# Kernel tuning notes

Hardware: AMD Instinct MI355X
Metric: run time of the kernel (lower is better)

Reference implementation:

```python
import jax, jax.numpy as jnp
import numpy as np

NB, NC, NT = 64, 128, 6
NEURON = (25, 50, 100)
AXIS = 4
EPS = 1e-12


def _offdiag_idx(nc):
    # static [nc, nc-1] column indices of the off-diagonal entries per row
    idx = np.tile(np.arange(nc)[None, :], (nc, 1))
    mask = ~np.eye(nc, dtype=bool)
    return idx[mask].reshape(nc, nc - 1)


def setup_inputs() -> dict:
    key = jax.random.key(0)
    ks = jax.random.split(key, 8)
    P = NT * NT
    coords = jax.random.normal(ks[0], (NB, NC, 3), dtype=jnp.float32)
    atom_types = jax.random.randint(ks[1], (NC,), 0, NT)
    dims = [1] + list(NEURON)
    inp = {"coords": coords, "atom_types": atom_types}
    for i in range(3):
        bound = 1.0 / float(np.sqrt(dims[i]))
        inp[f"W{i+1}"] = jax.random.uniform(ks[2 + 2 * i], (P, dims[i + 1], dims[i]), jnp.float32, -bound, bound)
        inp[f"b{i+1}"] = jax.random.uniform(ks[3 + 2 * i], (P, dims[i + 1]), jnp.float32, -bound, bound)
    return inp


def _channel_dense(x, W, b, channels, res_mode):
    # x: [nb, Ppairs, in]; W[channels]: [Ppairs, out, in] (redundant per-pair gather, as in torch)
    y = jnp.einsum('bpi,poi->bpo', x, W[channels]) + b[channels]
    y = jnp.tanh(y)
    if res_mode == 1:
        y = y + x
    elif res_mode == 2:
        y = y + jnp.concatenate([x, x], axis=-1)
    return y


def _forward(coords, atom_types, W1, b1, W2, b2, W3, b3):
    nb, nc, _ = coords.shape
    idx = jnp.asarray(_offdiag_idx(nc))  # [nc, nc-1], static
    row = jnp.arange(nc)[:, None]

    rij = coords[:, :, None, :] - coords[:, None, :, :]          # [nb,nc,nc,3]
    rij = rij[:, row, idx]                                       # [nb,nc,nc-1,3] off-diagonal
    dij = jnp.linalg.norm(rij, axis=-1)                          # [nb,nc,nc-1]
    dinv = 1.0 / jnp.maximum(dij, EPS)
    loc_env_r = dinv
    loc_env_a = rij * (dinv * dinv)[..., None]                   # [nb,nc,nc-1,3]

    neighbor_types = atom_types[idx]                             # [nc,nc-1]
    channels = (atom_types[:, None] * NT + neighbor_types).reshape(-1)  # [nc*(nc-1)]

    x = loc_env_r.reshape(nb, -1, 1)                             # [nb,P,1]
    y = _channel_dense(x, W1, b1, channels, res_mode=0)          # 1 -> 25
    y = _channel_dense(y, W2, b2, channels, res_mode=2)          # 25 -> 50 (+concat res)
    y = _channel_dense(y, W3, b3, channels, res_mode=2)          # 50 -> 100 (+concat res)

    out = y.reshape(nb, nc, nc - 1, NEURON[-1])                  # [nb,nc,k,100]
    t1 = jnp.einsum('bnka,bnkf->bnaf', loc_env_a, out[..., :AXIS])   # [nb,nc,3,4]
    t2 = jnp.einsum('bnka,bnaf->bnkf', loc_env_a, t1)                # [nb,nc,k,4]
    res = jnp.einsum('bnkg,bnkf->bngf', out, t2)                     # [nb,nc,100,4]
    return res.reshape(nb, nc, -1)


def reference(coords, atom_types, W1, b1, W2, b2, W3, b3):
    return _forward(coords, atom_types, W1, b1, W2, b2, W3, b3)
```

## Files before the change

kernel.cpp:

```cpp
#include <hip/hip_runtime.h>

#define NBATCH 64
#define NCH    128
#define NTYPE  6
#define NK     127
#define N1     25
#define N2     50
#define N3     100
#define NAXIS  4
#define OUTPER 400
#define W2P    28
#define MAXKP  152
#define MAXC4  38

#define R5(M)  M(0) M(1) M(2) M(3) M(4)
#define R7(M)  M(0) M(1) M(2) M(3) M(4) M(5) M(6)
#define R12(M) M(0) M(1) M(2) M(3) M(4) M(5) M(6) M(7) M(8) M(9) M(10) M(11)
#define R25(M) M(0) M(1) M(2) M(3) M(4) M(5) M(6) M(7) M(8) M(9) M(10) M(11) M(12) \
               M(13) M(14) M(15) M(16) M(17) M(18) M(19) M(20) M(21) M(22) M(23) M(24)
#define R25A(M,a) M(a,0) M(a,1) M(a,2) M(a,3) M(a,4) M(a,5) M(a,6) M(a,7) M(a,8) M(a,9) \
               M(a,10) M(a,11) M(a,12) M(a,13) M(a,14) M(a,15) M(a,16) M(a,17) M(a,18) \
               M(a,19) M(a,20) M(a,21) M(a,22) M(a,23) M(a,24)
#define R50(M) R25(M) M(25) M(26) M(27) M(28) M(29) M(30) M(31) M(32) M(33) M(34) \
               M(35) M(36) M(37) M(38) M(39) M(40) M(41) M(42) M(43) M(44) M(45) \
               M(46) M(47) M(48) M(49)

__device__ __forceinline__ float tanh_fast(float x) {
    float e = __expf(2.0f * x);
    return 1.0f - 2.0f * __builtin_amdgcn_rcpf(e + 1.0f);
}

__global__ void k_transpose(const float* __restrict__ coords, float* __restrict__ ct) {
    int t = blockIdx.x * blockDim.x + threadIdx.x;
    if (t >= NBATCH * NCH * 3) return;
    int b  = t & (NBATCH - 1);
    int jd = t >> 6;
    int d  = jd % 3;
    int j  = jd / 3;
    ct[t] = coords[(b * NCH + j) * 3 + d];
}

__device__ __forceinline__ void sort_k_by_type(
    const int* __restrict__ types, int n, int* tysh, int* ks, int* bins, int tid, int nthr)
{
    for (int t = tid; t < NCH; t += nthr) tysh[t] = types[t];
    __syncthreads();
    if (tid == 0) {
        for (int t = 0; t < NTYPE; ++t) bins[t] = 0;
        for (int k = 0; k < NK; ++k) { int j = (k < n) ? k : k + 1; bins[tysh[j]]++; }
        int off = 0;
        for (int t = 0; t < NTYPE; ++t) { int c = bins[t]; bins[t] = off; off += c; }
        for (int k = 0; k < NK; ++k) { int j = (k < n) ? k : k + 1; ks[bins[tysh[j]]++] = k; }
    }
    __syncthreads();
}

__device__ __forceinline__ void sort_pad(
    const int* __restrict__ types, int n, int* tysh, int* ksp, int* chs, int* aux,
    int tid, int nthr)
{
    for (int t = tid; t < NCH; t += nthr) tysh[t] = types[t];
    __syncthreads();
    if (tid == 0) {
        int cnt[NTYPE], pos[NTYPE];
        for (int t = 0; t < NTYPE; ++t) cnt[t] = 0;
        for (int k = 0; k < NK; ++k) { int j = (k < n) ? k : k + 1; cnt[tysh[j]]++; }
        int c = 0;
        for (int t = 0; t < NTYPE; ++t) {
            pos[t] = c;
            int pc = (cnt[t] + 3) & ~3;
            for (int q = c >> 2; q < (c + pc) >> 2; ++q) chs[q] = t;
            for (int p = c + cnt[t]; p < c + pc; ++p) ksp[p] = -1;
            c += pc;
        }
        aux[0] = c >> 2;
        for (int k = 0; k < NK; ++k) { int j = (k < n) ? k : k + 1; ksp[pos[tysh[j]]++] = k; }
    }
    __syncthreads();
}

__global__ __launch_bounds__(256, 4) void k_mlp(
    const float* __restrict__ ct, const int* __restrict__ types,
    const float* __restrict__ W1, const float* __restrict__ B1,
    const float* __restrict__ W2, const float* __restrict__ B2,
    const float* __restrict__ W3, const float* __restrict__ B3,
    float* __restrict__ t1buf)
{
    __shared__ int ks[NK];
    __shared__ int tysh[NCH];
    __shared__ int bins[NTYPE];

    const int n  = blockIdx.x >> 2;
    const int qc = blockIdx.x & 3;
    const int w  = threadIdx.x >> 6;
    const int b  = threadIdx.x & 63;
    const int k0 = qc * 32 + w * 8;

    sort_k_by_type(types, n, tysh, ks, bins, threadIdx.x, 256);

    const float cx = ct[(n*3+0)*NBATCH + b];
    const float cy = ct[(n*3+1)*NBATCH + b];
    const float cz = ct[(n*3+2)*NBATCH + b];
    const int tn = __builtin_amdgcn_readfirstlane(tysh[n]);

    float t1a[12];
#define TIN(i) t1a[i] = 0.0f;
    R12(TIN)
#undef TIN

    for (int kk = 0; kk < 8; ++kk) {
        const int kidx = k0 + kk;
        if (kidx >= NK) break;
        const int sk = __builtin_amdgcn_readfirstlane(ks[kidx]);
        const int j  = (sk < n) ? sk : sk + 1;
        const int ch = __builtin_amdgcn_readfirstlane(tn * NTYPE + tysh[j]);

        const float dx = cx - ct[(j*3+0)*NBATCH + b];
        const float dy = cy - ct[(j*3+1)*NBATCH + b];
        const float dz = cz - ct[(j*3+2)*NBATCH + b];
        const float d2 = dx*dx + dy*dy + dz*dz;
        const float dd = sqrtf(d2);
        const float dinv = __builtin_amdgcn_rcpf(fmaxf(dd, 1e-12f));
        const float di2 = dinv * dinv;
        const float ax = dx * di2, ay = dy * di2, az = dz * di2;

        const float* w1r = W1 + ch * N1;
        const float* b1r = B1 + ch * N1;
        float y1[N1];
#define L1S(o) y1[o] = tanh_fast(fmaf(dinv, w1r[o], b1r[o]));
        R25(L1S)
#undef L1S

        const float* w2r = W2 + ch * (N2 * N1);
        const float* b2r = B2 + ch * N2;
        const float* w3r = W3 + ch * (N3 * N2);
        float zf[4];
        zf[0] = B3[ch*N3+0]; zf[1] = B3[ch*N3+1];
        zf[2] = B3[ch*N3+2]; zf[3] = B3[ch*N3+3];
        float r[4];
#define MLP2I(o,i) z = fmaf(w2r[(o)*N1+(i)], y1[i], z);
#define MLP2(o) { float z = b2r[o]; R25A(MLP2I,o) \
        float y2o = tanh_fast(z) + y1[(o)%N1]; \
        if ((o) < 4) r[(o)&3] = y2o; \
        zf[0] = fmaf(w3r[0*N2+(o)], y2o, zf[0]); \
        zf[1] = fmaf(w3r[1*N2+(o)], y2o, zf[1]); \
        zf[2] = fmaf(w3r[2*N2+(o)], y2o, zf[2]); \
        zf[3] = fmaf(w3r[3*N2+(o)], y2o, zf[3]); }
        R50(MLP2)
#undef MLP2
#undef MLP2I

#define O4F(f) { float o4 = tanh_fast(zf[f]) + r[f]; \
        t1a[0+(f)] = fmaf(ax, o4, t1a[0+(f)]); \
        t1a[4+(f)] = fmaf(ay, o4, t1a[4+(f)]); \
        t1a[8+(f)] = fmaf(az, o4, t1a[8+(f)]); }
        O4F(0) O4F(1) O4F(2) O4F(3)
#undef O4F
    }

    float* dst = t1buf + (n * 12) * NBATCH + b;
#define TAT(i) atomicAdd(dst + (i) * NBATCH, t1a[i]);
    R12(TAT)
#undef TAT
}

__global__ __launch_bounds__(512, 3) void k_res2(
    const float* __restrict__ ct, const int* __restrict__ types,
    const float* __restrict__ W1, const float* __restrict__ B1,
    const float* __restrict__ W2, const float* __restrict__ B2,
    const float* __restrict__ W3, const float* __restrict__ B3,
    const float* __restrict__ t1buf, float* __restrict__ out)
{
    __shared__ float y2t[4 * N2 * NBATCH];
    __shared__ float t2s[4 * NBATCH * NAXIS];
    __shared__ float w2s[N2 * W2P];
    __shared__ float w1s[N1], b1s[N1], b2s[N2];
    __shared__ int   ksp[MAXKP];
    __shared__ int   chs[MAXC4];
    __shared__ int   tysh[NCH];
    __shared__ int   aux[1];

    const int n    = blockIdx.x >> 2;
    const int gh   = (blockIdx.x >> 1) & 1;
    const int kh   = blockIdx.x & 1;
    const int w    = threadIdx.x >> 6;
    const int lane = threadIdx.x & 63;
    const int kk2  = w >> 1;
    const int h    = w & 1;
    const int tid  = threadIdx.x;

    sort_pad(types, n, tysh, ksp, chs, aux, tid, 512);
    const int nch4 = __builtin_amdgcn_readfirstlane(aux[0]);
    const int c_lo = kh ? (nch4 >> 1) : 0;
    const int c_hi = kh ? nch4 : (nch4 >> 1);

    const int tn = __builtin_amdgcn_readfirstlane(tysh[n]);

    float t1r[12];
#define T1L(i) t1r[i] = t1buf[(n*12 + (i))*NBATCH + lane];
    R12(T1L)
#undef T1L

    const int g0 = __builtin_amdgcn_readfirstlane(w * 7);
    int gg[7];
#define GGI(gi) gg[gi] = ((g0 + (gi)) < N2) ? (g0 + (gi)) : (N2 - 1);
    R7(GGI)
#undef GGI

    float racc[7][4];
#define RIN(gi) racc[gi][0]=0.f; racc[gi][1]=0.f; racc[gi][2]=0.f; racc[gi][3]=0.f;
    R7(RIN)
#undef RIN

    float b3v[7];
    int prevty = -1;

    for (int kc = c_lo; kc < c_hi; ++kc) {
        const int tj = __builtin_amdgcn_readfirstlane(chs[kc]);
        const int ch = tn * NTYPE + tj;
        if (tj != prevty) {
            for (int idx = tid; idx < N2*N1; idx += 512)
                w2s[(idx / N1) * W2P + (idx % N1)] = W2[ch*(N2*N1) + idx];
            if (tid < N1) { w1s[tid] = W1[ch*N1+tid]; b1s[tid] = B1[ch*N1+tid]; }
            if (tid < N2) b2s[tid] = B2[ch*N2+tid];
#define B3L(gi) b3v[gi] = B3[ch*N3 + gh*N2 + gg[gi]];
            R7(B3L)
#undef B3L
            prevty = tj;
            __syncthreads();
        }
        const int kb = kc * 4;
        {
            const int sk = __builtin_amdgcn_readfirstlane(ksp[kb + kk2]);
            if (sk >= 0) {
                const int j = (sk < n) ? sk : sk + 1;
                const float dx = ct[(n*3+0)*NBATCH + lane] - ct[(j*3+0)*NBATCH + lane];
                const float dy = ct[(n*3+1)*NBATCH + lane] - ct[(j*3+1)*NBATCH + lane];
                const float dz = ct[(n*3+2)*NBATCH + lane] - ct[(j*3+2)*NBATCH + lane];
                const float d2 = dx*dx + dy*dy + dz*dz;
                const float dd = sqrtf(d2);
                const float dinv = __builtin_amdgcn_rcpf(fmaxf(dd, 1e-12f));

                if (h == 0) {
                    const float di2 = dinv * dinv;
                    const float ax = dx * di2, ay = dy * di2, az = dz * di2;
#define T2W(f) t2s[(kk2*NBATCH + lane)*NAXIS + (f)] = \
                    ax*t1r[f] + ay*t1r[4+(f)] + az*t1r[8+(f)];
                    T2W(0) T2W(1) T2W(2) T2W(3)
#undef T2W
                }

                float y1[N1];
#define L1S(o) y1[o] = tanh_fast(fmaf(dinv, w1s[o], b1s[o]));
                R25(L1S)
#undef L1S
                const int ob = h * N1;
                float* y2w = &y2t[(kk2*N2 + ob)*NBATCH + lane];
#define P1Q(oi,q) { float4 wq = *(const float4*)&w2s[(ob+(oi))*W2P + (q)*4]; \
                    z = fmaf(wq.x, y1[(q)*4+0], z); z = fmaf(wq.y, y1[(q)*4+1], z); \
                    z = fmaf(wq.z, y1[(q)*4+2], z); z = fmaf(wq.w, y1[(q)*4+3], z); }
#define P1S(oi) { float z = b2s[ob+(oi)]; \
                  P1Q(oi,0) P1Q(oi,1) P1Q(oi,2) P1Q(oi,3) P1Q(oi,4) P1Q(oi,5) \
                  z = fmaf(w2s[(ob+(oi))*W2P + 24], y1[24], z); \
                  y2w[(oi)*NBATCH] = tanh_fast(z) + y1[oi]; }
                R25(P1S)
#undef P1S
#undef P1Q
            }
        }
        __syncthreads();
        const float* w3b = W3 + ch * (N3*N2) + (gh*N2) * N2;
        for (int kp = 0; kp < 2; ++kp) {
            const int skA = __builtin_amdgcn_readfirstlane(ksp[kb + kp*2 + 0]);
            const int skB = __builtin_amdgcn_readfirstlane(ksp[kb + kp*2 + 1]);
            if (skA < 0 && skB < 0) continue;
            const float* y2A = &y2t[((kp*2+0)*N2)*NBATCH + lane];
            const float* y2B = &y2t[((kp*2+1)*N2)*NBATCH + lane];
            float zA[7], zB[7];
#define ZIN(gi) zA[gi] = b3v[gi]; zB[gi] = b3v[gi];
            R7(ZIN)
#undef ZIN
            for (int ic = 0; ic < 10; ++ic) {
                const int io = ic * 5;
                float w35[7][5];
#define W35L(gi) w35[gi][0]=w3b[gg[gi]*N2+io+0]; w35[gi][1]=w3b[gg[gi]*N2+io+1]; \
                 w35[gi][2]=w3b[gg[gi]*N2+io+2]; w35[gi][3]=w3b[gg[gi]*N2+io+3]; \
                 w35[gi][4]=w3b[gg[gi]*N2+io+4];
                R7(W35L)
#undef W35L
                if (skA >= 0) {
                    float yv[5];
#define LDA(i) yv[i] = y2A[(io + (i))*NBATCH];
                    R5(LDA)
#undef LDA
#define FA(gi) zA[gi]=fmaf(w35[gi][0],yv[0],zA[gi]); zA[gi]=fmaf(w35[gi][1],yv[1],zA[gi]); \
               zA[gi]=fmaf(w35[gi][2],yv[2],zA[gi]); zA[gi]=fmaf(w35[gi][3],yv[3],zA[gi]); \
               zA[gi]=fmaf(w35[gi][4],yv[4],zA[gi]);
                    R7(FA)
#undef FA
                }
                if (skB >= 0) {
                    float yv[5];
#define LDB(i) yv[i] = y2B[(io + (i))*NBATCH];
                    R5(LDB)
#undef LDB
#define FB(gi) zB[gi]=fmaf(w35[gi][0],yv[0],zB[gi]); zB[gi]=fmaf(w35[gi][1],yv[1],zB[gi]); \
               zB[gi]=fmaf(w35[gi][2],yv[2],zB[gi]); zB[gi]=fmaf(w35[gi][3],yv[3],zB[gi]); \
               zB[gi]=fmaf(w35[gi][4],yv[4],zB[gi]);
                    R7(FB)
#undef FB
                }
            }
            if (skA >= 0) {
                const float4 t2v = *(const float4*)&t2s[((kp*2+0)*NBATCH + lane)*NAXIS];
#define PFA(gi) { float o3 = tanh_fast(zA[gi]) + y2A[gg[gi]*NBATCH]; \
                  racc[gi][0] = fmaf(o3, t2v.x, racc[gi][0]); \
                  racc[gi][1] = fmaf(o3, t2v.y, racc[gi][1]); \
                  racc[gi][2] = fmaf(o3, t2v.z, racc[gi][2]); \
                  racc[gi][3] = fmaf(o3, t2v.w, racc[gi][3]); }
                R7(PFA)
#undef PFA
            }
            if (skB >= 0) {
                const float4 t2v = *(const float4*)&t2s[((kp*2+1)*NBATCH + lane)*NAXIS];
#define PFB(gi) { float o3 = tanh_fast(zB[gi]) + y2B[gg[gi]*NBATCH]; \
                  racc[gi][0] = fmaf(o3, t2v.x, racc[gi][0]); \
                  racc[gi][1] = fmaf(o3, t2v.y, racc[gi][1]); \
                  racc[gi][2] = fmaf(o3, t2v.z, racc[gi][2]); \
                  racc[gi][3] = fmaf(o3, t2v.w, racc[gi][3]); }
                R7(PFB)
#undef PFB
            }
        }
        __syncthreads();
    }

#define PST(gi) if (g0 + (gi) < N2) { \
        float* dp = &out[(lane*NCH + n)*OUTPER + (gh*N2 + g0 + (gi))*NAXIS]; \
        atomicAdd(dp + 0, racc[gi][0]); \
        atomicAdd(dp + 1, racc[gi][1]); \
        atomicAdd(dp + 2, racc[gi][2]); \
        atomicAdd(dp + 3, racc[gi][3]); }
    R7(PST)
#undef PST
}

extern "C" void kernel_launch(void* const* d_in, const int* in_sizes, int n_in,
                              void* d_out, int out_size, void* d_ws, size_t ws_size,
                              hipStream_t stream) {
    const float* coords = (const float*)d_in[0];
    const int*   types  = (const int*)d_in[1];
    const float* W1 = (const float*)d_in[2];
    const float* B1 = (const float*)d_in[3];
    const float* W2 = (const float*)d_in[4];
    const float* B2 = (const float*)d_in[5];
    const float* W3 = (const float*)d_in[6];
    const float* B3 = (const float*)d_in[7];
    float* out = (float*)d_out;

    float* t1buf = (float*)d_ws;
    float* ct    = t1buf + NCH * 12 * NBATCH;

    hipMemsetAsync(t1buf, 0, (size_t)NCH * 12 * NBATCH * sizeof(float), stream);
    hipMemsetAsync(out, 0, (size_t)out_size * sizeof(float), stream);

    k_transpose<<<(NBATCH*NCH*3 + 255)/256, 256, 0, stream>>>(coords, ct);
    k_mlp <<<NCH*4, 256, 0, stream>>>(ct, types, W1,B1,W2,B2,W3,B3, t1buf);
    k_res2<<<NCH*4, 512, 0, stream>>>(ct, types, W1,B1,W2,B2,W3,B3, t1buf, out);
}
```

Before: 829.2 us.

## Process four neighbors per W3 load with float4-packed y2 layout in layer 3

```diff
diff --git a/kernel.cpp b/kernel.cpp
--- a/kernel.cpp
+++ b/kernel.cpp
@@ -12,6 +12,7 @@
 #define W2P    28
 #define MAXKP  152
 #define MAXC4  38
+#define NQ     13
 
 #define R5(M)  M(0) M(1) M(2) M(3) M(4)
 #define R7(M)  M(0) M(1) M(2) M(3) M(4) M(5) M(6)
@@ -164,14 +165,14 @@
 #undef TAT
 }
 
-__global__ __launch_bounds__(512, 3) void k_res2(
+__global__ __launch_bounds__(512, 4) void k_res2(
     const float* __restrict__ ct, const int* __restrict__ types,
     const float* __restrict__ W1, const float* __restrict__ B1,
     const float* __restrict__ W2, const float* __restrict__ B2,
     const float* __restrict__ W3, const float* __restrict__ B3,
     const float* __restrict__ t1buf, float* __restrict__ out)
 {
-    __shared__ float y2t[4 * N2 * NBATCH];
+    __shared__ float y2t[4 * NQ * NBATCH * 4];
     __shared__ float t2s[4 * NBATCH * NAXIS];
     __shared__ float w2s[N2 * W2P];
     __shared__ float w1s[N1], b1s[N1], b2s[N2];
@@ -179,6 +180,8 @@
     __shared__ int   chs[MAXC4];
     __shared__ int   tysh[NCH];
     __shared__ int   aux[1];
+
+#define Y2I(k,q,b,j) ((((k)*NQ + (q))*NBATCH + (b))*4 + (j))
 
     const int n    = blockIdx.x >> 2;
     const int gh   = (blockIdx.x >> 1) & 1;
@@ -195,6 +198,10 @@
     const int c_hi = kh ? nch4 : (nch4 >> 1);
 
     const int tn = __builtin_amdgcn_readfirstlane(tysh[n]);
+
+    const float cx = ct[(n*3+0)*NBATCH + lane];
+    const float cy = ct[(n*3+1)*NBATCH + lane];
+    const float cz = ct[(n*3+2)*NBATCH + lane];
 
     float t1r[12];
 #define T1L(i) t1r[i] = t1buf[(n*12 + (i))*NBATCH + lane];
@@ -234,9 +241,9 @@
             const int sk = __builtin_amdgcn_readfirstlane(ksp[kb + kk2]);
             if (sk >= 0) {
                 const int j = (sk < n) ? sk : sk + 1;
-                const float dx = ct[(n*3+0)*NBATCH + lane] - ct[(j*3+0)*NBATCH + lane];
-                const float dy = ct[(n*3+1)*NBATCH + lane] - ct[(j*3+1)*NBATCH + lane];
-                const float dz = ct[(n*3+2)*NBATCH + lane] - ct[(j*3+2)*NBATCH + lane];
+                const float dx = cx - ct[(j*3+0)*NBATCH + lane];
+                const float dy = cy - ct[(j*3+1)*NBATCH + lane];
+                const float dz = cz - ct[(j*3+2)*NBATCH + lane];
                 const float d2 = dx*dx + dy*dy + dz*dz;
                 const float dd = sqrtf(d2);
                 const float dinv = __builtin_amdgcn_rcpf(fmaxf(dd, 1e-12f));
@@ -244,10 +251,12 @@
                 if (h == 0) {
                     const float di2 = dinv * dinv;
                     const float ax = dx * di2, ay = dy * di2, az = dz * di2;
-#define T2W(f) t2s[(kk2*NBATCH + lane)*NAXIS + (f)] = \
-                    ax*t1r[f] + ay*t1r[4+(f)] + az*t1r[8+(f)];
-                    T2W(0) T2W(1) T2W(2) T2W(3)
-#undef T2W
+                    float4 t2v;
+                    t2v.x = ax*t1r[0] + ay*t1r[4] + az*t1r[8];
+                    t2v.y = ax*t1r[1] + ay*t1r[5] + az*t1r[9];
+                    t2v.z = ax*t1r[2] + ay*t1r[6] + az*t1r[10];
+                    t2v.w = ax*t1r[3] + ay*t1r[7] + az*t1r[11];
+                    *(float4*)&t2s[(kk2*NBATCH + lane)*NAXIS] = t2v;
                 }
 
                 float y1[N1];
@@ -255,82 +264,111 @@
                 R25(L1S)
 #undef L1S
                 const int ob = h * N1;
-                float* y2w = &y2t[(kk2*N2 + ob)*NBATCH + lane];
+                float yo[N1];
 #define P1Q(oi,q) { float4 wq = *(const float4*)&w2s[(ob+(oi))*W2P + (q)*4]; \
                     z = fmaf(wq.x, y1[(q)*4+0], z); z = fmaf(wq.y, y1[(q)*4+1], z); \
                     z = fmaf(wq.z, y1[(q)*4+2], z); z = fmaf(wq.w, y1[(q)*4+3], z); }
 #define P1S(oi) { float z = b2s[ob+(oi)]; \
                   P1Q(oi,0) P1Q(oi,1) P1Q(oi,2) P1Q(oi,3) P1Q(oi,4) P1Q(oi,5) \
                   z = fmaf(w2s[(ob+(oi))*W2P + 24], y1[24], z); \
-                  y2w[(oi)*NBATCH] = tanh_fast(z) + y1[oi]; }
-                R25(P1S)
+                  yo[oi] = tanh_fast(z) + y1[oi]; }
+#define ST4(q,a0,a1,a2,a3) { float4 v; v.x=(a0); v.y=(a1); v.z=(a2); v.w=(a3); \
+                  *(float4*)&y2t[Y2I(kk2,(q),lane,0)] = v; }
+                P1S(0) P1S(1) P1S(2) P1S(3)
+                if (h == 0) { ST4(0, yo[0],yo[1],yo[2],yo[3]) }
+                else { y2t[Y2I(kk2,6,lane,1)] = yo[0];
+                       y2t[Y2I(kk2,6,lane,2)] = yo[1];
+                       y2t[Y2I(kk2,6,lane,3)] = yo[2]; }
+                P1S(4) P1S(5) P1S(6) P1S(7)
+                if (h == 0) { ST4(1, yo[4],yo[5],yo[6],yo[7]) }
+                else        { ST4(7, yo[3],yo[4],yo[5],yo[6]) }
+                P1S(8) P1S(9) P1S(10) P1S(11)
+                if (h == 0) { ST4(2, yo[8],yo[9],yo[10],yo[11]) }
+                else        { ST4(8, yo[7],yo[8],yo[9],yo[10]) }
+                P1S(12) P1S(13) P1S(14) P1S(15)
+                if (h == 0) { ST4(3, yo[12],yo[13],yo[14],yo[15]) }
+                else        { ST4(9, yo[11],yo[12],yo[13],yo[14]) }
+                P1S(16) P1S(17) P1S(18) P1S(19)
+                if (h == 0) { ST4(4, yo[16],yo[17],yo[18],yo[19]) }
+                else        { ST4(10, yo[15],yo[16],yo[17],yo[18]) }
+                P1S(20) P1S(21) P1S(22) P1S(23)
+                if (h == 0) { ST4(5, yo[20],yo[21],yo[22],yo[23]) }
+                else        { ST4(11, yo[19],yo[20],yo[21],yo[22]) }
+                P1S(24)
+                if (h == 0) { y2t[Y2I(kk2,6,lane,0)] = yo[24]; }
+                else        { ST4(12, yo[23],yo[24],0.0f,0.0f) }
+#undef ST4
 #undef P1S
 #undef P1Q
+            } else {
+                const float4 zv = make_float4(0.f, 0.f, 0.f, 0.f);
+                if (h == 0) {
+                    *(float4*)&t2s[(kk2*NBATCH + lane)*NAXIS] = zv;
+                    for (int q = 0; q < 7; ++q)
+                        *(float4*)&y2t[Y2I(kk2,q,lane,0)] = zv;
+                } else {
+                    for (int q = 7; q < NQ; ++q)
+                        *(float4*)&y2t[Y2I(kk2,q,lane,0)] = zv;
+                }
             }
         }
         __syncthreads();
-        const float* w3b = W3 + ch * (N3*N2) + (gh*N2) * N2;
-        for (int kp = 0; kp < 2; ++kp) {
-            const int skA = __builtin_amdgcn_readfirstlane(ksp[kb + kp*2 + 0]);
-            const int skB = __builtin_amdgcn_readfirstlane(ksp[kb + kp*2 + 1]);
-            if (skA < 0 && skB < 0) continue;
-            const float* y2A = &y2t[((kp*2+0)*N2)*NBATCH + lane];
-            const float* y2B = &y2t[((kp*2+1)*N2)*NBATCH + lane];
-            float zA[7], zB[7];
-#define ZIN(gi) zA[gi] = b3v[gi]; zB[gi] = b3v[gi];
+        {
+            const float* w3r[7];
+#define W3RI(gi) w3r[gi] = W3 + ((size_t)ch*N3 + gh*N2 + gg[gi])*N2;
+            R7(W3RI)
+#undef W3RI
+            float z0[7], z1[7], z2[7], z3[7];
+#define ZIN(gi) z0[gi]=b3v[gi]; z1[gi]=b3v[gi]; z2[gi]=b3v[gi]; z3[gi]=b3v[gi];
             R7(ZIN)
 #undef ZIN
-            for (int ic = 0; ic < 10; ++ic) {
-                const int io = ic * 5;
-                float w35[7][5];
-#define W35L(gi) w35[gi][0]=w3b[gg[gi]*N2+io+0]; w35[gi][1]=w3b[gg[gi]*N2+io+1]; \
-                 w35[gi][2]=w3b[gg[gi]*N2+io+2]; w35[gi][3]=w3b[gg[gi]*N2+io+3]; \
-                 w35[gi][4]=w3b[gg[gi]*N2+io+4];
-                R7(W35L)
-#undef W35L
-                if (skA >= 0) {
-                    float yv[5];
-#define LDA(i) yv[i] = y2A[(io + (i))*NBATCH];
-                    R5(LDA)
-#undef LDA
-#define FA(gi) zA[gi]=fmaf(w35[gi][0],yv[0],zA[gi]); zA[gi]=fmaf(w35[gi][1],yv[1],zA[gi]); \
-               zA[gi]=fmaf(w35[gi][2],yv[2],zA[gi]); zA[gi]=fmaf(w35[gi][3],yv[3],zA[gi]); \
-               zA[gi]=fmaf(w35[gi][4],yv[4],zA[gi]);
-                    R7(FA)
-#undef FA
-                }
-                if (skB >= 0) {
-                    float yv[5];
-#define LDB(i) yv[i] = y2B[(io + (i))*NBATCH];
-                    R5(LDB)
-#undef LDB
-#define FB(gi) zB[gi]=fmaf(w35[gi][0],yv[0],zB[gi]); zB[gi]=fmaf(w35[gi][1],yv[1],zB[gi]); \
-               zB[gi]=fmaf(w35[gi][2],yv[2],zB[gi]); zB[gi]=fmaf(w35[gi][3],yv[3],zB[gi]); \
-               zB[gi]=fmaf(w35[gi][4],yv[4],zB[gi]);
-                    R7(FB)
-#undef FB
-                }
+#pragma unroll 2
+            for (int iq = 0; iq < 12; ++iq) {
+                const int io = iq * 4;
+                float wa[7], wb[7], wc[7], wd[7];
+#define WLD(gi) { wa[gi]=w3r[gi][io+0]; wb[gi]=w3r[gi][io+1]; \
+                  wc[gi]=w3r[gi][io+2]; wd[gi]=w3r[gi][io+3]; }
+                R7(WLD)
+#undef WLD
+                const float4 yv0 = *(const float4*)&y2t[Y2I(0, iq, lane, 0)];
+                const float4 yv1 = *(const float4*)&y2t[Y2I(1, iq, lane, 0)];
+                const float4 yv2 = *(const float4*)&y2t[Y2I(2, iq, lane, 0)];
+                const float4 yv3 = *(const float4*)&y2t[Y2I(3, iq, lane, 0)];
+#define FK(gi) \
+  z0[gi]=fmaf(wd[gi],yv0.w,fmaf(wc[gi],yv0.z,fmaf(wb[gi],yv0.y,fmaf(wa[gi],yv0.x,z0[gi])))); \
+  z1[gi]=fmaf(wd[gi],yv1.w,fmaf(wc[gi],yv1.z,fmaf(wb[gi],yv1.y,fmaf(wa[gi],yv1.x,z1[gi])))); \
+  z2[gi]=fmaf(wd[gi],yv2.w,fmaf(wc[gi],yv2.z,fmaf(wb[gi],yv2.y,fmaf(wa[gi],yv2.x,z2[gi])))); \
+  z3[gi]=fmaf(wd[gi],yv3.w,fmaf(wc[gi],yv3.z,fmaf(wb[gi],yv3.y,fmaf(wa[gi],yv3.x,z3[gi]))));
+                R7(FK)
+#undef FK
             }
-            if (skA >= 0) {
-                const float4 t2v = *(const float4*)&t2s[((kp*2+0)*NBATCH + lane)*NAXIS];
-#define PFA(gi) { float o3 = tanh_fast(zA[gi]) + y2A[gg[gi]*NBATCH]; \
-                  racc[gi][0] = fmaf(o3, t2v.x, racc[gi][0]); \
-                  racc[gi][1] = fmaf(o3, t2v.y, racc[gi][1]); \
-                  racc[gi][2] = fmaf(o3, t2v.z, racc[gi][2]); \
-                  racc[gi][3] = fmaf(o3, t2v.w, racc[gi][3]); }
-                R7(PFA)
-#undef PFA
+            {
+                float wa[7], wb[7];
+#define WLE(gi) { wa[gi]=w3r[gi][48]; wb[gi]=w3r[gi][49]; }
+                R7(WLE)
+#undef WLE
+                const float4 yv0 = *(const float4*)&y2t[Y2I(0, 12, lane, 0)];
+                const float4 yv1 = *(const float4*)&y2t[Y2I(1, 12, lane, 0)];
+                const float4 yv2 = *(const float4*)&y2t[Y2I(2, 12, lane, 0)];
+                const float4 yv3 = *(const float4*)&y2t[Y2I(3, 12, lane, 0)];
+#define FE(gi) \
+  z0[gi]=fmaf(wb[gi],yv0.y,fmaf(wa[gi],yv0.x,z0[gi])); \
+  z1[gi]=fmaf(wb[gi],yv1.y,fmaf(wa[gi],yv1.x,z1[gi])); \
+  z2[gi]=fmaf(wb[gi],yv2.y,fmaf(wa[gi],yv2.x,z2[gi])); \
+  z3[gi]=fmaf(wb[gi],yv3.y,fmaf(wa[gi],yv3.x,z3[gi]));
+                R7(FE)
+#undef FE
             }
-            if (skB >= 0) {
-                const float4 t2v = *(const float4*)&t2s[((kp*2+1)*NBATCH + lane)*NAXIS];
-#define PFB(gi) { float o3 = tanh_fast(zB[gi]) + y2B[gg[gi]*NBATCH]; \
-                  racc[gi][0] = fmaf(o3, t2v.x, racc[gi][0]); \
-                  racc[gi][1] = fmaf(o3, t2v.y, racc[gi][1]); \
-                  racc[gi][2] = fmaf(o3, t2v.z, racc[gi][2]); \
-                  racc[gi][3] = fmaf(o3, t2v.w, racc[gi][3]); }
-                R7(PFB)
-#undef PFB
-            }
+#define PFG(kq, gi, Z) { \
+    const float res = y2t[Y2I(kq, (gg[gi]>>2), lane, (gg[gi]&3))]; \
+    const float o3 = tanh_fast(Z[gi]) + res; \
+    racc[gi][0]=fmaf(o3,t2v.x,racc[gi][0]); racc[gi][1]=fmaf(o3,t2v.y,racc[gi][1]); \
+    racc[gi][2]=fmaf(o3,t2v.z,racc[gi][2]); racc[gi][3]=fmaf(o3,t2v.w,racc[gi][3]); }
+#define PFK(kq, Z) { const float4 t2v = *(const float4*)&t2s[((kq)*NBATCH + lane)*NAXIS]; \
+    PFG(kq,0,Z) PFG(kq,1,Z) PFG(kq,2,Z) PFG(kq,3,Z) PFG(kq,4,Z) PFG(kq,5,Z) PFG(kq,6,Z) }
+            PFK(0, z0) PFK(1, z1) PFK(2, z2) PFK(3, z3)
+#undef PFK
+#undef PFG
         }
         __syncthreads();
     }
@@ -343,6 +381,7 @@
         atomicAdd(dp + 3, racc[gi][3]); }
     R7(PST)
 #undef PST
+#undef Y2I
 }
 
 extern "C" void kernel_launch(void* const* d_in, const int* in_sizes, int n_in,
```

Result: slower. 1.010 ms (+21.8%).

## Widen k_res2 to 1024 threads covering both output halves per block

Applied to the files above, without the earlier changes.

```diff
diff --git a/kernel.cpp b/kernel.cpp
--- a/kernel.cpp
+++ b/kernel.cpp
@@ -164,7 +164,7 @@
 #undef TAT
 }
 
-__global__ __launch_bounds__(512, 3) void k_res2(
+__global__ __launch_bounds__(1024, 1) void k_res2(
     const float* __restrict__ ct, const int* __restrict__ types,
     const float* __restrict__ W1, const float* __restrict__ B1,
     const float* __restrict__ W2, const float* __restrict__ B2,
@@ -181,18 +181,19 @@
     __shared__ int   aux[1];
 
     const int n    = blockIdx.x >> 2;
-    const int gh   = (blockIdx.x >> 1) & 1;
-    const int kh   = blockIdx.x & 1;
+    const int kh   = blockIdx.x & 3;
     const int w    = threadIdx.x >> 6;
     const int lane = threadIdx.x & 63;
-    const int kk2  = w >> 1;
-    const int h    = w & 1;
+    const int kk2  = w >> 2;
+    const int sub  = w & 3;
+    const int h    = sub >> 1;
+    const int q    = sub & 1;
     const int tid  = threadIdx.x;
 
-    sort_pad(types, n, tysh, ksp, chs, aux, tid, 512);
+    sort_pad(types, n, tysh, ksp, chs, aux, tid, 1024);
     const int nch4 = __builtin_amdgcn_readfirstlane(aux[0]);
-    const int c_lo = kh ? (nch4 >> 1) : 0;
-    const int c_hi = kh ? nch4 : (nch4 >> 1);
+    const int c_lo = (nch4 * kh) >> 2;
+    const int c_hi = (nch4 * (kh + 1)) >> 2;
 
     const int tn = __builtin_amdgcn_readfirstlane(tysh[n]);
 
@@ -201,7 +202,8 @@
     R12(T1L)
 #undef T1L
 
-    const int g0 = __builtin_amdgcn_readfirstlane(w * 7);
+    const int ghw = w >> 3;
+    const int g0  = __builtin_amdgcn_readfirstlane((w & 7) * 7);
     int gg[7];
 #define GGI(gi) gg[gi] = ((g0 + (gi)) < N2) ? (g0 + (gi)) : (N2 - 1);
     R7(GGI)
@@ -219,11 +221,11 @@
         const int tj = __builtin_amdgcn_readfirstlane(chs[kc]);
         const int ch = tn * NTYPE + tj;
         if (tj != prevty) {
-            for (int idx = tid; idx < N2*N1; idx += 512)
+            for (int idx = tid; idx < N2*N1; idx += 1024)
                 w2s[(idx / N1) * W2P + (idx % N1)] = W2[ch*(N2*N1) + idx];
             if (tid < N1) { w1s[tid] = W1[ch*N1+tid]; b1s[tid] = B1[ch*N1+tid]; }
             if (tid < N2) b2s[tid] = B2[ch*N2+tid];
-#define B3L(gi) b3v[gi] = B3[ch*N3 + gh*N2 + gg[gi]];
+#define B3L(gi) b3v[gi] = B3[ch*N3 + ghw*N2 + gg[gi]];
             R7(B3L)
 #undef B3L
             prevty = tj;
@@ -241,7 +243,7 @@
                 const float dd = sqrtf(d2);
                 const float dinv = __builtin_amdgcn_rcpf(fmaxf(dd, 1e-12f));
 
-                if (h == 0) {
+                if (sub == 0) {
                     const float di2 = dinv * dinv;
                     const float ax = dx * di2, ay = dy * di2, az = dz * di2;
 #define T2W(f) t2s[(kk2*NBATCH + lane)*NAXIS + (f)] = \
@@ -254,22 +256,31 @@
 #define L1S(o) y1[o] = tanh_fast(fmaf(dinv, w1s[o], b1s[o]));
                 R25(L1S)
 #undef L1S
-                const int ob = h * N1;
-                float* y2w = &y2t[(kk2*N2 + ob)*NBATCH + lane];
-#define P1Q(oi,q) { float4 wq = *(const float4*)&w2s[(ob+(oi))*W2P + (q)*4]; \
-                    z = fmaf(wq.x, y1[(q)*4+0], z); z = fmaf(wq.y, y1[(q)*4+1], z); \
-                    z = fmaf(wq.z, y1[(q)*4+2], z); z = fmaf(wq.w, y1[(q)*4+3], z); }
-#define P1S(oi) { float z = b2s[ob+(oi)]; \
-                  P1Q(oi,0) P1Q(oi,1) P1Q(oi,2) P1Q(oi,3) P1Q(oi,4) P1Q(oi,5) \
-                  z = fmaf(w2s[(ob+(oi))*W2P + 24], y1[24], z); \
-                  y2w[(oi)*NBATCH] = tanh_fast(z) + y1[oi]; }
-                R25(P1S)
-#undef P1S
+                const int o0 = h * N1 + q * 13;
+                float* y2w = &y2t[(kk2*N2 + o0)*NBATCH + lane];
+                const float* w2row0 = &w2s[o0 * W2P];
+#define P1Q(r,qq) { float4 wq = *(const float4*)&w2row0[(r)*W2P + (qq)*4]; \
+                    z = fmaf(wq.x, y1[(qq)*4+0], z); z = fmaf(wq.y, y1[(qq)*4+1], z); \
+                    z = fmaf(wq.z, y1[(qq)*4+2], z); z = fmaf(wq.w, y1[(qq)*4+3], z); }
+#define P1SQ(r,YI) { float z = b2s[o0+(r)]; \
+                  P1Q(r,0) P1Q(r,1) P1Q(r,2) P1Q(r,3) P1Q(r,4) P1Q(r,5) \
+                  z = fmaf(w2row0[(r)*W2P + 24], y1[24], z); \
+                  y2w[(r)*NBATCH] = tanh_fast(z) + y1[YI]; }
+                if (q == 0) {
+                    P1SQ(0,0)  P1SQ(1,1)  P1SQ(2,2)  P1SQ(3,3)  P1SQ(4,4)
+                    P1SQ(5,5)  P1SQ(6,6)  P1SQ(7,7)  P1SQ(8,8)  P1SQ(9,9)
+                    P1SQ(10,10) P1SQ(11,11) P1SQ(12,12)
+                } else {
+                    P1SQ(0,13) P1SQ(1,14) P1SQ(2,15) P1SQ(3,16) P1SQ(4,17)
+                    P1SQ(5,18) P1SQ(6,19) P1SQ(7,20) P1SQ(8,21) P1SQ(9,22)
+                    P1SQ(10,23) P1SQ(11,24)
+                }
+#undef P1SQ
 #undef P1Q
             }
         }
         __syncthreads();
-        const float* w3b = W3 + ch * (N3*N2) + (gh*N2) * N2;
+        const float* w3b = W3 + ch * (N3*N2) + (ghw*N2) * N2;
         for (int kp = 0; kp < 2; ++kp) {
             const int skA = __builtin_amdgcn_readfirstlane(ksp[kb + kp*2 + 0]);
             const int skB = __builtin_amdgcn_readfirstlane(ksp[kb + kp*2 + 1]);
@@ -336,7 +347,7 @@
     }
 
 #define PST(gi) if (g0 + (gi) < N2) { \
-        float* dp = &out[(lane*NCH + n)*OUTPER + (gh*N2 + g0 + (gi))*NAXIS]; \
+        float* dp = &out[(lane*NCH + n)*OUTPER + (ghw*N2 + g0 + (gi))*NAXIS]; \
         atomicAdd(dp + 0, racc[gi][0]); \
         atomicAdd(dp + 1, racc[gi][1]); \
         atomicAdd(dp + 2, racc[gi][2]); \
@@ -366,5 +377,5 @@
 
     k_transpose<<<(NBATCH*NCH*3 + 255)/256, 256, 0, stream>>>(coords, ct);
     k_mlp <<<NCH*4, 256, 0, stream>>>(ct, types, W1,B1,W2,B2,W3,B3, t1buf);
-    k_res2<<<NCH*4, 512, 0, stream>>>(ct, types, W1,B1,W2,B2,W3,B3, t1buf, out);
-}
+    k_res2<<<NCH*4, 1024, 0, stream>>>(ct, types, W1,B1,W2,B2,W3,B3, t1buf, out);
+}
```

Result: slower. 1.277 ms (+54.0%).

## Process neighbor pairs per wave in k_mlp to share weight loads

Applied to the files above, without the earlier changes.

```diff
diff --git a/kernel.cpp b/kernel.cpp
--- a/kernel.cpp
+++ b/kernel.cpp
@@ -12,6 +12,8 @@
 #define W2P    28
 #define MAXKP  152
 #define MAXC4  38
+#define MAXKP2 136
+#define MAXC2  68
 
 #define R5(M)  M(0) M(1) M(2) M(3) M(4)
 #define R7(M)  M(0) M(1) M(2) M(3) M(4) M(5) M(6)
@@ -40,17 +42,26 @@
     ct[t] = coords[(b * NCH + j) * 3 + d];
 }
 
-__device__ __forceinline__ void sort_k_by_type(
-    const int* __restrict__ types, int n, int* tysh, int* ks, int* bins, int tid, int nthr)
+__device__ __forceinline__ void sort_pad2(
+    const int* __restrict__ types, int n, int* tysh, int* ksp, int* chs, int* aux,
+    int tid, int nthr)
 {
     for (int t = tid; t < NCH; t += nthr) tysh[t] = types[t];
     __syncthreads();
     if (tid == 0) {
-        for (int t = 0; t < NTYPE; ++t) bins[t] = 0;
-        for (int k = 0; k < NK; ++k) { int j = (k < n) ? k : k + 1; bins[tysh[j]]++; }
-        int off = 0;
-        for (int t = 0; t < NTYPE; ++t) { int c = bins[t]; bins[t] = off; off += c; }
-        for (int k = 0; k < NK; ++k) { int j = (k < n) ? k : k + 1; ks[bins[tysh[j]]++] = k; }
+        int cnt[NTYPE], pos[NTYPE];
+        for (int t = 0; t < NTYPE; ++t) cnt[t] = 0;
+        for (int k = 0; k < NK; ++k) { int j = (k < n) ? k : k + 1; cnt[tysh[j]]++; }
+        int c = 0;
+        for (int t = 0; t < NTYPE; ++t) {
+            pos[t] = c;
+            int pc = (cnt[t] + 1) & ~1;
+            for (int q = c >> 1; q < (c + pc) >> 1; ++q) chs[q] = t;
+            for (int p = c + cnt[t]; p < c + pc; ++p) ksp[p] = -1;
+            c += pc;
+        }
+        aux[0] = c >> 1;
+        for (int k = 0; k < NK; ++k) { int j = (k < n) ? k : k + 1; ksp[pos[tysh[j]]++] = k; }
     }
     __syncthreads();
 }
@@ -79,24 +90,26 @@
     __syncthreads();
 }
 
-__global__ __launch_bounds__(256, 4) void k_mlp(
+__global__ __launch_bounds__(256, 2) void k_mlp(
     const float* __restrict__ ct, const int* __restrict__ types,
     const float* __restrict__ W1, const float* __restrict__ B1,
     const float* __restrict__ W2, const float* __restrict__ B2,
     const float* __restrict__ W3, const float* __restrict__ B3,
     float* __restrict__ t1buf)
 {
-    __shared__ int ks[NK];
+    __shared__ int ksp[MAXKP2];
+    __shared__ int chs[MAXC2];
     __shared__ int tysh[NCH];
-    __shared__ int bins[NTYPE];
+    __shared__ int aux[1];
 
     const int n  = blockIdx.x >> 2;
     const int qc = blockIdx.x & 3;
     const int w  = threadIdx.x >> 6;
     const int b  = threadIdx.x & 63;
-    const int k0 = qc * 32 + w * 8;
-
-    sort_k_by_type(types, n, tysh, ks, bins, threadIdx.x, 256);
+    const int wv = qc * 4 + w;
+
+    sort_pad2(types, n, tysh, ksp, chs, aux, threadIdx.x, 256);
+    const int npair = __builtin_amdgcn_readfirstlane(aux[0]);
 
     const float cx = ct[(n*3+0)*NBATCH + b];
     const float cy = ct[(n*3+1)*NBATCH + b];
@@ -108,54 +121,81 @@
     R12(TIN)
 #undef TIN
 
-    for (int kk = 0; kk < 8; ++kk) {
-        const int kidx = k0 + kk;
-        if (kidx >= NK) break;
-        const int sk = __builtin_amdgcn_readfirstlane(ks[kidx]);
-        const int j  = (sk < n) ? sk : sk + 1;
-        const int ch = __builtin_amdgcn_readfirstlane(tn * NTYPE + tysh[j]);
-
-        const float dx = cx - ct[(j*3+0)*NBATCH + b];
-        const float dy = cy - ct[(j*3+1)*NBATCH + b];
-        const float dz = cz - ct[(j*3+2)*NBATCH + b];
-        const float d2 = dx*dx + dy*dy + dz*dz;
-        const float dd = sqrtf(d2);
-        const float dinv = __builtin_amdgcn_rcpf(fmaxf(dd, 1e-12f));
-        const float di2 = dinv * dinv;
-        const float ax = dx * di2, ay = dy * di2, az = dz * di2;
+    for (int pp = 0; pp < 5; ++pp) {
+        const int P = pp * 16 + wv;
+        if (P >= npair) break;
+        const int skA  = __builtin_amdgcn_readfirstlane(ksp[2*P]);
+        const int skBr = __builtin_amdgcn_readfirstlane(ksp[2*P + 1]);
+        const int haveB = (skBr >= 0);
+        const int skB = haveB ? skBr : skA;
+        const int ch  = __builtin_amdgcn_readfirstlane(tn * NTYPE + chs[P]);
+
+        const int jA = (skA < n) ? skA : skA + 1;
+        const int jB = (skB < n) ? skB : skB + 1;
+
+        const float dxA = cx - ct[(jA*3+0)*NBATCH + b];
+        const float dyA = cy - ct[(jA*3+1)*NBATCH + b];
+        const float dzA = cz - ct[(jA*3+2)*NBATCH + b];
+        const float ddA = sqrtf(dxA*dxA + dyA*dyA + dzA*dzA);
+        const float dinvA = __builtin_amdgcn_rcpf(fmaxf(ddA, 1e-12f));
+        const float di2A = dinvA * dinvA;
+        const float axA = dxA*di2A, ayA = dyA*di2A, azA = dzA*di2A;
+
+        const float dxB = cx - ct[(jB*3+0)*NBATCH + b];
+        const float dyB = cy - ct[(jB*3+1)*NBATCH + b];
+        const float dzB = cz - ct[(jB*3+2)*NBATCH + b];
+        const float ddB = sqrtf(dxB*dxB + dyB*dyB + dzB*dzB);
+        const float dinvB = __builtin_amdgcn_rcpf(fmaxf(ddB, 1e-12f));
+        const float di2B = dinvB * dinvB;
+        const float axB = dxB*di2B, ayB = dyB*di2B, azB = dzB*di2B;
 
         const float* w1r = W1 + ch * N1;
         const float* b1r = B1 + ch * N1;
-        float y1[N1];
-#define L1S(o) y1[o] = tanh_fast(fmaf(dinv, w1r[o], b1r[o]));
-        R25(L1S)
-#undef L1S
+        float y1A[N1], y1B[N1];
+#define L1P(o) { const float w1o = w1r[o], b1o = b1r[o]; \
+                 y1A[o] = tanh_fast(fmaf(dinvA, w1o, b1o)); \
+                 y1B[o] = tanh_fast(fmaf(dinvB, w1o, b1o)); }
+        R25(L1P)
+#undef L1P
 
         const float* w2r = W2 + ch * (N2 * N1);
         const float* b2r = B2 + ch * N2;
         const float* w3r = W3 + ch * (N3 * N2);
-        float zf[4];
-        zf[0] = B3[ch*N3+0]; zf[1] = B3[ch*N3+1];
-        zf[2] = B3[ch*N3+2]; zf[3] = B3[ch*N3+3];
-        float r[4];
-#define MLP2I(o,i) z = fmaf(w2r[(o)*N1+(i)], y1[i], z);
-#define MLP2(o) { float z = b2r[o]; R25A(MLP2I,o) \
-        float y2o = tanh_fast(z) + y1[(o)%N1]; \
-        if ((o) < 4) r[(o)&3] = y2o; \
-        zf[0] = fmaf(w3r[0*N2+(o)], y2o, zf[0]); \
-        zf[1] = fmaf(w3r[1*N2+(o)], y2o, zf[1]); \
-        zf[2] = fmaf(w3r[2*N2+(o)], y2o, zf[2]); \
-        zf[3] = fmaf(w3r[3*N2+(o)], y2o, zf[3]); }
-        R50(MLP2)
-#undef MLP2
-#undef MLP2I
-
-#define O4F(f) { float o4 = tanh_fast(zf[f]) + r[f]; \
-        t1a[0+(f)] = fmaf(ax, o4, t1a[0+(f)]); \
-        t1a[4+(f)] = fmaf(ay, o4, t1a[4+(f)]); \
-        t1a[8+(f)] = fmaf(az, o4, t1a[8+(f)]); }
-        O4F(0) O4F(1) O4F(2) O4F(3)
-#undef O4F
+        float zfA[4], zfB[4];
+        zfA[0] = B3[ch*N3+0]; zfA[1] = B3[ch*N3+1];
+        zfA[2] = B3[ch*N3+2]; zfA[3] = B3[ch*N3+3];
+        zfB[0] = zfA[0]; zfB[1] = zfA[1]; zfB[2] = zfA[2]; zfB[3] = zfA[3];
+        float rA[4], rB[4];
+#define M2I(o,i) { const float w2v = w2r[(o)*N1+(i)]; \
+                   zA = fmaf(w2v, y1A[i], zA); zB = fmaf(w2v, y1B[i], zB); }
+#define M2(o) { float zA = b2r[o]; float zB = zA; R25A(M2I,o) \
+        const float y2A_ = tanh_fast(zA) + y1A[(o)%N1]; \
+        const float y2B_ = tanh_fast(zB) + y1B[(o)%N1]; \
+        if ((o) < 4) { rA[(o)&3] = y2A_; rB[(o)&3] = y2B_; } \
+        { const float w30 = w3r[0*N2+(o)], w31 = w3r[1*N2+(o)]; \
+          const float w32 = w3r[2*N2+(o)], w33 = w3r[3*N2+(o)]; \
+          zfA[0] = fmaf(w30, y2A_, zfA[0]); zfB[0] = fmaf(w30, y2B_, zfB[0]); \
+          zfA[1] = fmaf(w31, y2A_, zfA[1]); zfB[1] = fmaf(w31, y2B_, zfB[1]); \
+          zfA[2] = fmaf(w32, y2A_, zfA[2]); zfB[2] = fmaf(w32, y2B_, zfB[2]); \
+          zfA[3] = fmaf(w33, y2A_, zfA[3]); zfB[3] = fmaf(w33, y2B_, zfB[3]); } }
+        R50(M2)
+#undef M2
+#undef M2I
+
+#define O4A(f) { const float o4 = tanh_fast(zfA[f]) + rA[f]; \
+        t1a[0+(f)] = fmaf(axA, o4, t1a[0+(f)]); \
+        t1a[4+(f)] = fmaf(ayA, o4, t1a[4+(f)]); \
+        t1a[8+(f)] = fmaf(azA, o4, t1a[8+(f)]); }
+        O4A(0) O4A(1) O4A(2) O4A(3)
+#undef O4A
+        if (haveB) {
+#define O4B(f) { const float o4 = tanh_fast(zfB[f]) + rB[f]; \
+        t1a[0+(f)] = fmaf(axB, o4, t1a[0+(f)]); \
+        t1a[4+(f)] = fmaf(ayB, o4, t1a[4+(f)]); \
+        t1a[8+(f)] = fmaf(azB, o4, t1a[8+(f)]); }
+            O4B(0) O4B(1) O4B(2) O4B(3)
+#undef O4B
+        }
     }
 
     float* dst = t1buf + (n * 12) * NBATCH + b;
```

New measurement: 887.3 us. +7.0%, slower.
